# Kernel optimization log

Hardware: AMD Instinct MI355X
Metric: run time of the kernel (lower is better)

## Reference

```python
import jax, jax.numpy as jnp
import numpy as np

D_MODEL = 1024
NUM_HEADS = 16
D_K = D_MODEL // NUM_HEADS


def setup_inputs() -> dict:
    key = jax.random.key(0)
    ks = jax.random.split(key, 6)
    B, S = 2, 2048
    scale = 1.0 / np.sqrt(D_MODEL)
    x = jax.random.normal(ks[0], (B, S, D_MODEL), dtype=jnp.float32)
    w_q = jax.random.normal(ks[1], (D_MODEL, D_MODEL), dtype=jnp.float32) * scale
    w_k = jax.random.normal(ks[2], (D_MODEL, D_MODEL), dtype=jnp.float32) * scale
    w_v = jax.random.normal(ks[3], (D_MODEL, D_MODEL), dtype=jnp.float32) * scale
    w_o = jax.random.normal(ks[4], (D_MODEL, D_MODEL), dtype=jnp.float32) * scale
    b_o = jax.random.normal(ks[5], (D_MODEL,), dtype=jnp.float32) * 0.01
    return {"x": x, "w_q": w_q, "w_k": w_k, "w_v": w_v, "w_o": w_o, "b_o": b_o}


def reference(x, w_q, w_k, w_v, w_o, b_o):
    B, S, _ = x.shape
    # Linear(d, d, bias=False): y = x @ W.T ; weights stored torch-style [out, in]
    def proj(w):
        y = jnp.einsum('bsd,ed->bse', x, w)
        return y.reshape(B, S, NUM_HEADS, D_K).transpose(0, 2, 1, 3)  # [B,H,S,Dk]
    Q, K, V = proj(w_q), proj(w_k), proj(w_v)
    scores = jnp.einsum('bhqd,bhkd->bhqk', Q, K) / np.sqrt(D_K)
    attn = jax.nn.softmax(scores, axis=-1)  # dropout p=0 (eval) -> identity
    out = jnp.einsum('bhqk,bhkd->bhqd', attn, V)
    out = out.transpose(0, 2, 1, 3).reshape(B, S, D_MODEL)
    return jnp.einsum('bsd,ed->bse', out, w_o) + b_o
```

## Files before the change

kernel.cpp:

```cpp
#include <hip/hip_runtime.h>
#include <hip/hip_bf16.h>


typedef __bf16 bf16x8 __attribute__((ext_vector_type(8)));
typedef float f32x4 __attribute__((ext_vector_type(4)));
typedef float f32x16 __attribute__((ext_vector_type(16)));

__device__ __forceinline__ unsigned short f2bf(float f) {
  union { float f; unsigned int u; } c; c.f = f;
  unsigned int u = c.u;
  return (unsigned short)((u + 0x7FFFu + ((u >> 16) & 1u)) >> 16);
}

__device__ __forceinline__ unsigned int cvtpk(float a, float b) {
  unsigned int r;
  asm("v_cvt_pk_bf16_f32 %0, %1, %2" : "=v"(r) : "v"(a), "v"(b));
  return r;
}

__device__ __forceinline__ bf16x8 ld_frag(const unsigned short* p) {
  union { uint4 u; bf16x8 b; } c;
  c.u = *(const uint4*)p;
  return c.b;
}

__device__ __forceinline__ uint4 cvt8(const float* __restrict__ p) {
  float4 a = *(const float4*)p;
  float4 b = *(const float4*)(p + 4);
  union { uint4 u; unsigned short s[8]; } r;
  r.s[0] = f2bf(a.x); r.s[1] = f2bf(a.y); r.s[2] = f2bf(a.z); r.s[3] = f2bf(a.w);
  r.s[4] = f2bf(b.x); r.s[5] = f2bf(b.y); r.s[6] = f2bf(b.z); r.s[7] = f2bf(b.w);
  return r.u;
}

typedef __attribute__((address_space(1))) const unsigned int as1_u32;
typedef __attribute__((address_space(3))) unsigned int as3_u32;
__device__ __forceinline__ void async16(const unsigned short* g,
                                        unsigned short* l) {
  __builtin_amdgcn_global_load_lds(
      (as1_u32*)(unsigned long long)g,
      (as3_u32*)(unsigned int)(unsigned long long)l, 16, 0, 0);
}

__global__ __launch_bounds__(256) void cvt_all(
    const float* __restrict__ s0, const float* __restrict__ s1,
    const float* __restrict__ s2, const float* __restrict__ s3,
    const float* __restrict__ s4,
    unsigned short* __restrict__ d0, unsigned short* __restrict__ d1,
    unsigned short* __restrict__ d2, unsigned short* __restrict__ d3,
    unsigned short* __restrict__ d4) {
  const float* srcs[5] = {s0, s1, s2, s3, s4};
  unsigned short* dsts[5] = {d0, d1, d2, d3, d4};
  const int ns[5] = {4194304, 1048576, 1048576, 1048576, 1048576};
  const int y = blockIdx.y;
  const int idx = (blockIdx.x * 256 + threadIdx.x) * 8;
  if (idx >= ns[y]) return;
  *(uint4*)(dsts[y] + idx) = cvt8(srcs[y] + idx);
}

template <int BM, bool OUT_F32>
__global__ __launch_bounds__(256, 3) void gemm_bt(
    const unsigned short* __restrict__ A,
    const unsigned short* __restrict__ w0,
    const unsigned short* __restrict__ w1,
    const unsigned short* __restrict__ w2,
    const float* __restrict__ bias,
    void* __restrict__ outraw, float z0scale) {
  constexpr int NT = (BM == 128) ? 4 : 2;
  constexpr int RA = BM / 4;
  const int z = blockIdx.z;
  const unsigned short* W = (z == 0) ? w0 : ((z == 1) ? w1 : w2);
  const float scl = (z == 0) ? z0scale : 1.0f;

  __shared__ unsigned short smem[(BM + 128) * 64];
  unsigned short* a_lds = smem;
  unsigned short* b_lds = smem + BM * 64;

  const int tid = threadIdx.x;
  const int wave = tid >> 6, lane = tid & 63;
  const int quad = lane >> 4, l16 = lane & 15;
  const int wm = (BM == 128) ? (wave >> 1) * 64 : 0;
  const int wn = (BM == 128) ? (wave & 1) * 64 : wave * 32;
  const int bm = blockIdx.x * BM, bn = blockIdx.y * 128;

  const int r8 = lane >> 3;
  const int sl = (lane & 7) ^ r8;
  const unsigned short* ga = A + (size_t)(bm + wave * RA + r8) * 1024 + sl * 8;
  const unsigned short* gb = W + (size_t)(bn + wave * 32 + r8) * 1024 + sl * 8;
  unsigned short* la = &a_lds[wave * RA * 64];
  unsigned short* lb = &b_lds[wave * 32 * 64];

  f32x4 acc[4][NT] = {};

  for (int k0 = 0; k0 < 1024; k0 += 64) {
#pragma unroll
    for (int c = 0; c < RA / 8; ++c)
      async16(ga + (size_t)c * 8 * 1024, la + c * 512);
#pragma unroll
    for (int c = 0; c < 4; ++c)
      async16(gb + (size_t)c * 8 * 1024, lb + c * 512);
    ga += 64; gb += 64;
    __syncthreads();

    bf16x8 af[2][4], bfr[2][NT];
#pragma unroll
    for (int kk = 0; kk < 2; ++kk) {
#pragma unroll
      for (int t = 0; t < 4; ++t) {
        const int row = wm + t * 16 + l16;
        af[kk][t] =
            ld_frag(&a_lds[row * 64 + (((kk * 4 + quad) ^ (row & 7)) * 8)]);
      }
#pragma unroll
      for (int t = 0; t < NT; ++t) {
        const int row = wn + t * 16 + l16;
        bfr[kk][t] =
            ld_frag(&b_lds[row * 64 + (((kk * 4 + quad) ^ (row & 7)) * 8)]);
      }
    }
#pragma unroll
    for (int kk = 0; kk < 2; ++kk)
#pragma unroll
      for (int mt = 0; mt < 4; ++mt)
#pragma unroll
        for (int nt = 0; nt < NT; ++nt)
          acc[mt][nt] = __builtin_amdgcn_mfma_f32_16x16x32_bf16(
              af[kk][mt], bfr[kk][nt], acc[mt][nt], 0, 0, 0);
    __syncthreads();
  }

  if (!OUT_F32 && BM == 128 && z == 2) {
    unsigned short* tt = smem;
#pragma unroll
    for (int nt = 0; nt < NT; ++nt) {
      const int nl = wn + nt * 16 + l16;
#pragma unroll
      for (int mt = 0; mt < 4; ++mt) {
        const int ml = wm + mt * 16 + quad * 4;
        union { uint2 u; unsigned short s[4]; } pk;
#pragma unroll
        for (int r = 0; r < 4; ++r) pk.s[r] = f2bf(acc[mt][nt][r]);
        const int g = (ml >> 3) ^ (nl & 7);
        *(uint2*)&tt[nl * 128 + g * 8 + (ml & 7)] = pk.u;
      }
    }
    __syncthreads();
    const int nl = tid >> 1, sc = (tid & 1) * 64;
    const int bb = bm >> 11, s0 = bm & 2047;
    const int hh = (bn >> 6) + (nl >> 6);
    unsigned short* vtp = (unsigned short*)outraw + (size_t)2 * 4096 * 1024 +
                          ((size_t)(bb * 16 + hh)) * 131072 +
                          (size_t)(nl & 63) * 2048 + s0 + sc;
#pragma unroll
    for (int k = 0; k < 8; ++k) {
      const int g = ((sc + k * 8) >> 3) ^ (nl & 7);
      *(uint4*)&vtp[k * 8] = *(const uint4*)&tt[nl * 128 + g * 8];
    }
    return;
  }

#pragma unroll
  for (int nt = 0; nt < NT; ++nt) {
    const int n = bn + wn + nt * 16 + l16;
    const float bv = bias ? bias[n] : 0.0f;
#pragma unroll
    for (int mt = 0; mt < 4; ++mt)
#pragma unroll
      for (int r = 0; r < 4; ++r) {
        const int m = bm + wm + mt * 16 + quad * 4 + r;
        const float v = acc[mt][nt][r] * scl + bv;
        if (OUT_F32)
          ((float*)outraw)[(size_t)z * 4096 * 1024 + (size_t)m * 1024 + n] = v;
        else
          ((unsigned short*)outraw)[(size_t)z * 4096 * 1024 +
                                    (size_t)m * 1024 + n] = f2bf(v);
      }
  }
}

__global__ __launch_bounds__(256, 4) void attn4(
    const unsigned short* __restrict__ qkv,
    const unsigned short* __restrict__ vt_g,
    unsigned short* __restrict__ ab) {
  constexpr size_t PL = (size_t)4096 * 1024;
  const int qt = blockIdx.x, bh = blockIdx.y;
  const int b = bh >> 4, h = bh & 15;

  __shared__ __align__(16) unsigned short kvs[2][2][64 * 64];
  __shared__ float sm_l[2][2][32];

  const int tid = threadIdx.x;
  const int wave = tid >> 6, lane = tid & 63;
  const int ws = wave >> 1, wq = wave & 1;
  const int hi = lane >> 5, l32 = lane & 31;
  const int row8 = lane >> 3;
  const int sl = (lane & 7) ^ (row8 & 7);
  const int swz = (l32 & 7) * 8;

  const unsigned short* qrow =
      qkv + (size_t)(b * 2048 + qt * 64 + wq * 32 + l32) * 1024 + h * 64 +
      hi * 8;
  bf16x8 qf[4];
#pragma unroll
  for (int kc = 0; kc < 4; ++kc) qf[kc] = ld_frag(qrow + kc * 16);

  const unsigned short* gK =
      qkv + PL + (size_t)(b * 2048 + ws * 1024 + wq * 32 + row8) * 1024 +
      h * 64 + sl * 8;
  const unsigned short* gV =
      vt_g + (size_t)bh * 64 * 2048 + (size_t)(wq * 32 + row8) * 2048 +
      ws * 1024 + sl * 8;
  unsigned short* lK = &kvs[ws][0][wq * 4 * 512];
  unsigned short* lV = &kvs[ws][1][wq * 4 * 512];

  f32x16 o_acc[2] = {};
  float l_part = 0.0f;

  for (int t = 0; t < 16; ++t) {
#pragma unroll
    for (int c = 0; c < 4; ++c) {
      async16(gK + (size_t)c * 8 * 1024, lK + c * 512);
      async16(gV + (size_t)c * 8 * 2048, lV + c * 512);
    }
    gK += 64 * 1024;
    gV += 64;
    __syncthreads();

    f32x16 st[2] = {};
#pragma unroll
    for (int mb = 0; mb < 2; ++mb)
#pragma unroll
      for (int kc = 0; kc < 4; ++kc) {
        bf16x8 ak = ld_frag(
            &kvs[ws][0][(mb * 32 + l32) * 64 + (((2 * kc + hi) * 8) ^ swz)]);
        st[mb] = __builtin_amdgcn_mfma_f32_32x32x16_bf16(ak, qf[kc], st[mb],
                                                         0, 0, 0);
      }

    unsigned int u[2][4][2];
#pragma unroll
    for (int mb = 0; mb < 2; ++mb) {
#pragma unroll
      for (int r = 0; r < 16; ++r) {
        const float p = __builtin_amdgcn_exp2f(st[mb][r]);
        st[mb][r] = p;
        l_part += p;
      }
#pragma unroll
      for (int g = 0; g < 4; ++g) {
        u[mb][g][0] = cvtpk(st[mb][g * 4 + 0], st[mb][g * 4 + 1]);
        u[mb][g][1] = cvtpk(st[mb][g * 4 + 2], st[mb][g * 4 + 3]);
      }
    }

#pragma unroll
    for (int ks = 0; ks < 4; ++ks) {
      const int m = ks >> 1, g = (ks & 1) * 2;
      unsigned int a0 = u[m][g][0], b0 = u[m][g + 1][0];
      unsigned int a1 = u[m][g][1], b1 = u[m][g + 1][1];
      asm("v_permlane32_swap_b32 %0, %1" : "+v"(a0), "+v"(b0));
      asm("v_permlane32_swap_b32 %0, %1" : "+v"(a1), "+v"(b1));
      union { unsigned int w[4]; bf16x8 f; } pa;
      pa.w[0] = a0; pa.w[1] = a1; pa.w[2] = b0; pa.w[3] = b1;
#pragma unroll
      for (int nb = 0; nb < 2; ++nb) {
        bf16x8 bv = ld_frag(
            &kvs[ws][1][(nb * 32 + l32) * 64 + (((2 * ks + hi) * 8) ^ swz)]);
        o_acc[nb] = __builtin_amdgcn_mfma_f32_32x32x16_bf16(pa.f, bv,
                                                            o_acc[nb], 0, 0, 0);
      }
    }
    __syncthreads();
  }

  float lsum = l_part + __shfl_xor(l_part, 32);

  float* sm_o = (float*)&kvs[0][0][0];
  if (ws == 1) {
#pragma unroll
    for (int nb = 0; nb < 2; ++nb)
#pragma unroll
      for (int r = 0; r < 16; ++r) {
        const int q = (r & 3) + 8 * (r >> 2) + 4 * hi;
        sm_o[wq * 2048 + q * 64 + nb * 32 + l32] = o_acc[nb][r];
      }
  }
  if (lane < 32) sm_l[ws][wq][l32] = lsum;
  __syncthreads();

  if (ws == 0) {
#pragma unroll
    for (int r = 0; r < 16; ++r) {
      const int q = (r & 3) + 8 * (r >> 2) + 4 * hi;
      const float inv = 1.0f / (sm_l[0][wq][q] + sm_l[1][wq][q]);
      const size_t row = (size_t)(b * 2048 + qt * 64 + wq * 32 + q);
#pragma unroll
      for (int nb = 0; nb < 2; ++nb) {
        const float v =
            (o_acc[nb][r] + sm_o[wq * 2048 + q * 64 + nb * 32 + l32]) * inv;
        ab[row * 1024 + h * 64 + nb * 32 + l32] = f2bf(v);
      }
    }
  }
}

extern "C" void kernel_launch(void* const* d_in, const int* in_sizes, int n_in,
                              void* d_out, int out_size, void* d_ws,
                              size_t ws_size, hipStream_t stream) {
  const float* x  = (const float*)d_in[0];
  const float* wq = (const float*)d_in[1];
  const float* wk = (const float*)d_in[2];
  const float* wv = (const float*)d_in[3];
  const float* wo = (const float*)d_in[4];
  const float* bo = (const float*)d_in[5];

  constexpr size_t PL = (size_t)4096 * 1024;
  unsigned short* qkv = (unsigned short*)d_ws;
  unsigned short* xb  = qkv + 3 * PL;
  unsigned short* ab  = xb;
  unsigned short* wqb = qkv + 4 * PL;
  unsigned short* wkb = wqb + 1024 * 1024;
  unsigned short* wvb = wkb + 1024 * 1024;
  unsigned short* wob = wvb + 1024 * 1024;

  const float QSCALE = 0.18033688011112042f;

  cvt_all<<<dim3(2048, 5), 256, 0, stream>>>(x, wq, wk, wv, wo,
                                             xb, wqb, wkb, wvb, wob);
  gemm_bt<128, false><<<dim3(32, 8, 3), 256, 0, stream>>>(
      xb, wqb, wkb, wvb, nullptr, qkv, QSCALE);
  attn4<<<dim3(32, 32), 256, 0, stream>>>(qkv, qkv + 2 * PL, ab);
  gemm_bt<128, true><<<dim3(32, 8, 1), 256, 0, stream>>>(
      ab, wob, wob, wob, bo, d_out, 1.0f);
}
```

Measured before the change: 179.7 us.

## Double-buffer K/V tiles in attention with 32-key steps and prefetch

Reworks the attention kernel to use two LDS buffers, processing 32 keys per iteration instead of 64. The next K/V tile is prefetched asynchronously while the current one is used, so global loads overlap with MFMA work. It also adds a new V-tile swizzle for the narrower layout. The cost is twice as many iterations and barriers, each with less work, which leaves less compute to hide latency behind.

```diff
diff --git a/kernel.cpp b/kernel.cpp
--- a/kernel.cpp
+++ b/kernel.cpp
@@ -178,7 +178,7 @@
   }
 }
 
-__global__ __launch_bounds__(256, 4) void attn4(
+__global__ __launch_bounds__(256, 4) void attn7(
     const unsigned short* __restrict__ qkv,
     const unsigned short* __restrict__ vt_g,
     unsigned short* __restrict__ ab) {
@@ -186,16 +186,16 @@
   const int qt = blockIdx.x, bh = blockIdx.y;
   const int b = bh >> 4, h = bh & 15;
 
-  __shared__ __align__(16) unsigned short kvs[2][2][64 * 64];
+  __shared__ __align__(16) unsigned short kbuf[2][2][32 * 64];
+  __shared__ __align__(16) unsigned short vbuf[2][2][64 * 32];
   __shared__ float sm_l[2][2][32];
 
   const int tid = threadIdx.x;
   const int wave = tid >> 6, lane = tid & 63;
   const int ws = wave >> 1, wq = wave & 1;
   const int hi = lane >> 5, l32 = lane & 31;
-  const int row8 = lane >> 3;
-  const int sl = (lane & 7) ^ (row8 & 7);
   const int swz = (l32 & 7) * 8;
+  const int vswz = (l32 >> 1) & 3;
 
   const unsigned short* qrow =
       qkv + (size_t)(b * 2048 + qt * 64 + wq * 32 + l32) * 1024 + h * 64 +
@@ -204,78 +204,93 @@
 #pragma unroll
   for (int kc = 0; kc < 4; ++kc) qf[kc] = ld_frag(qrow + kc * 16);
 
+  const int krow8 = lane >> 3;
+  const int ksl = (lane & 7) ^ krow8;
   const unsigned short* gK =
-      qkv + PL + (size_t)(b * 2048 + ws * 1024 + wq * 32 + row8) * 1024 +
-      h * 64 + sl * 8;
+      qkv + PL + (size_t)(b * 2048 + ws * 1024 + wq * 16 + krow8) * 1024 +
+      h * 64 + ksl * 8;
+  const int vrow16 = lane >> 2;
+  const int vsl = (lane & 3) ^ ((lane >> 3) & 3);
   const unsigned short* gV =
-      vt_g + (size_t)bh * 64 * 2048 + (size_t)(wq * 32 + row8) * 2048 +
-      ws * 1024 + sl * 8;
-  unsigned short* lK = &kvs[ws][0][wq * 4 * 512];
-  unsigned short* lV = &kvs[ws][1][wq * 4 * 512];
+      vt_g + (size_t)bh * 64 * 2048 + (size_t)(wq * 32 + vrow16) * 2048 +
+      ws * 1024 + vsl * 8;
 
   f32x16 o_acc[2] = {};
   float l_part = 0.0f;
 
-  for (int t = 0; t < 16; ++t) {
-#pragma unroll
-    for (int c = 0; c < 4; ++c) {
-      async16(gK + (size_t)c * 8 * 1024, lK + c * 512);
-      async16(gV + (size_t)c * 8 * 2048, lV + c * 512);
-    }
-    gK += 64 * 1024;
-    gV += 64;
-    __syncthreads();
-
-    f32x16 st[2] = {};
-#pragma unroll
-    for (int mb = 0; mb < 2; ++mb)
-#pragma unroll
-      for (int kc = 0; kc < 4; ++kc) {
-        bf16x8 ak = ld_frag(
-            &kvs[ws][0][(mb * 32 + l32) * 64 + (((2 * kc + hi) * 8) ^ swz)]);
-        st[mb] = __builtin_amdgcn_mfma_f32_32x32x16_bf16(ak, qf[kc], st[mb],
-                                                         0, 0, 0);
-      }
-
-    unsigned int u[2][4][2];
-#pragma unroll
-    for (int mb = 0; mb < 2; ++mb) {
-#pragma unroll
-      for (int r = 0; r < 16; ++r) {
-        const float p = __builtin_amdgcn_exp2f(st[mb][r]);
-        st[mb][r] = p;
-        l_part += p;
-      }
-#pragma unroll
-      for (int g = 0; g < 4; ++g) {
-        u[mb][g][0] = cvtpk(st[mb][g * 4 + 0], st[mb][g * 4 + 1]);
-        u[mb][g][1] = cvtpk(st[mb][g * 4 + 2], st[mb][g * 4 + 3]);
-      }
-    }
-
-#pragma unroll
-    for (int ks = 0; ks < 4; ++ks) {
-      const int m = ks >> 1, g = (ks & 1) * 2;
-      unsigned int a0 = u[m][g][0], b0 = u[m][g + 1][0];
-      unsigned int a1 = u[m][g][1], b1 = u[m][g + 1][1];
+#pragma unroll
+  for (int c = 0; c < 2; ++c) {
+    async16(gK + (size_t)c * 8 * 1024, &kbuf[0][ws][wq * 1024 + c * 512]);
+    async16(gV + (size_t)c * 16 * 2048, &vbuf[0][ws][wq * 1024 + c * 512]);
+  }
+  gK += 32 * 1024;
+  gV += 32;
+  asm volatile("s_waitcnt vmcnt(0)" ::: "memory");
+  __builtin_amdgcn_s_barrier();
+  __builtin_amdgcn_sched_barrier(0);
+
+  for (int t = 0; t < 32; ++t) {
+    const int cur = t & 1, nxt = cur ^ 1;
+
+    if (t < 31) {
+#pragma unroll
+      for (int c = 0; c < 2; ++c) {
+        async16(gK + (size_t)c * 8 * 1024,
+                &kbuf[nxt][ws][wq * 1024 + c * 512]);
+        async16(gV + (size_t)c * 16 * 2048,
+                &vbuf[nxt][ws][wq * 1024 + c * 512]);
+      }
+      gK += 32 * 1024;
+      gV += 32;
+    }
+
+    f32x16 st = {};
+#pragma unroll
+    for (int kc = 0; kc < 4; ++kc) {
+      bf16x8 ak =
+          ld_frag(&kbuf[cur][ws][l32 * 64 + (((2 * kc + hi) * 8) ^ swz)]);
+      st = __builtin_amdgcn_mfma_f32_32x32x16_bf16(ak, qf[kc], st, 0, 0, 0);
+    }
+
+    unsigned int u[4][2];
+#pragma unroll
+    for (int r = 0; r < 16; ++r) {
+      const float p = __builtin_amdgcn_exp2f(st[r]);
+      st[r] = p;
+      l_part += p;
+    }
+#pragma unroll
+    for (int g = 0; g < 4; ++g) {
+      u[g][0] = cvtpk(st[g * 4 + 0], st[g * 4 + 1]);
+      u[g][1] = cvtpk(st[g * 4 + 2], st[g * 4 + 3]);
+    }
+
+#pragma unroll
+    for (int ks = 0; ks < 2; ++ks) {
+      unsigned int a0 = u[2 * ks][0], b0 = u[2 * ks + 1][0];
+      unsigned int a1 = u[2 * ks][1], b1 = u[2 * ks + 1][1];
       asm("v_permlane32_swap_b32 %0, %1" : "+v"(a0), "+v"(b0));
       asm("v_permlane32_swap_b32 %0, %1" : "+v"(a1), "+v"(b1));
       union { unsigned int w[4]; bf16x8 f; } pa;
       pa.w[0] = a0; pa.w[1] = a1; pa.w[2] = b0; pa.w[3] = b1;
 #pragma unroll
       for (int nb = 0; nb < 2; ++nb) {
-        bf16x8 bv = ld_frag(
-            &kvs[ws][1][(nb * 32 + l32) * 64 + (((2 * ks + hi) * 8) ^ swz)]);
+        const int d = nb * 32 + l32;
+        bf16x8 bv =
+            ld_frag(&vbuf[cur][ws][d * 32 + (((2 * ks + hi) ^ vswz) * 8)]);
         o_acc[nb] = __builtin_amdgcn_mfma_f32_32x32x16_bf16(pa.f, bv,
                                                             o_acc[nb], 0, 0, 0);
       }
     }
-    __syncthreads();
+
+    asm volatile("s_waitcnt vmcnt(0)" ::: "memory");
+    __builtin_amdgcn_s_barrier();
+    __builtin_amdgcn_sched_barrier(0);
   }
 
   float lsum = l_part + __shfl_xor(l_part, 32);
 
-  float* sm_o = (float*)&kvs[0][0][0];
+  float* sm_o = (float*)&kbuf[0][0][0];
   if (ws == 1) {
 #pragma unroll
     for (int nb = 0; nb < 2; ++nb)
@@ -329,7 +344,7 @@
                                              xb, wqb, wkb, wvb, wob);
   gemm_bt<128, false><<<dim3(32, 8, 3), 256, 0, stream>>>(
       xb, wqb, wkb, wvb, nullptr, qkv, QSCALE);
-  attn4<<<dim3(32, 32), 256, 0, stream>>>(qkv, qkv + 2 * PL, ab);
+  attn7<<<dim3(32, 32), 256, 0, stream>>>(qkv, qkv + 2 * PL, ab);
   gemm_bt<128, true><<<dim3(32, 8, 1), 256, 0, stream>>>(
       ab, wob, wob, wob, bo, d_out, 1.0f);
 }
```

Result: no change. 180.7 us (+0.6%).
